# Optimization experiments

Hardware: AMD Instinct MI355X
Metric: run time of the kernel (lower is better)

## Reference

```python
import jax, jax.numpy as jnp
import numpy as np

D, H, S, T, NN, IN_CH, FEAT, SPA, OUT, NL, FF, E = 512, 8, 64, 32, 512, 32, 64, 32, 32, 4, 2048, 16384
NEG = 0.2  # leaky relu negative slope (GATv2 default and alpha)

def _ln(x, g, b):
    m = x.mean(-1, keepdims=True)
    v = ((x - m) ** 2).mean(-1, keepdims=True)
    return (x - m) / jnp.sqrt(v + 1e-5) * g + b

def _posenc(L):
    pos = jnp.arange(L, dtype=jnp.float32)[:, None]
    div = jnp.exp(-jnp.log(10000.0) * jnp.arange(0, D, 2, dtype=jnp.float32) / D)
    pe = jnp.zeros((L, D), jnp.float32)
    pe = pe.at[:, 0::2].set(jnp.sin(pos * div)).at[:, 1::2].set(jnp.cos(pos * div))
    return pe[:, None, :]  # (L,1,D), seq-first

def _mha(xq, xkv, wqkv, bqkv, wo, bo, mask=None):
    Lq, N, _ = xq.shape
    Lk = xkv.shape[0]
    dh = D // H
    wq, wk, wv = jnp.split(wqkv, 3, axis=1)
    bq, bk, bv = jnp.split(bqkv, 3)
    q = (xq @ wq + bq).reshape(Lq, N, H, dh)
    k = (xkv @ wk + bk).reshape(Lk, N, H, dh)
    v = (xkv @ wv + bv).reshape(Lk, N, H, dh)
    s = jnp.einsum('qnhd,knhd->nhqk', q, k) / jnp.sqrt(jnp.float32(dh))
    if mask is not None:
        s = s + mask
    a = jax.nn.softmax(s, -1)
    o = jnp.einsum('nhqk,knhd->qnhd', a, v).reshape(Lq, N, D)
    return o @ wo + bo

def _gatv2(x, wl, wr, bl, br, att, bias, e_src, e_dst):
    # GATv2: e_ij = a . leakyrelu(Wl x_j + Wr x_i); softmax over incoming edges of i; out_i = sum alpha_ij Wl x_j
    n = x.shape[0]
    h, c = att.shape
    xl = (x @ wl + bl).reshape(n, h, c)
    xr = (x @ wr + br).reshape(n, h, c)
    z = jax.nn.leaky_relu(xl[e_src] + xr[e_dst], NEG)   # (E,H,C)
    e = jnp.einsum('ehc,hc->eh', z, att)                # (E,H)
    m = jax.lax.stop_gradient(jax.ops.segment_max(e, e_dst, num_segments=n))
    ex = jnp.exp(e - m[e_dst])
    den = jax.ops.segment_sum(ex, e_dst, num_segments=n)
    alpha = ex / den[e_dst]
    out = jax.ops.segment_sum(alpha[..., None] * xl[e_src], e_dst, num_segments=n)
    return out.reshape(n, h * c) + bias

def _fwd(src, tgt, w_enc_in, b_enc_in, w_dec_in, b_dec_in, w_map, b_map,
         enc_qkv_w, enc_qkv_b, enc_out_w, enc_out_b, enc_ff1_w, enc_ff1_b, enc_ff2_w, enc_ff2_b,
         enc_ln1_g, enc_ln1_b, enc_ln2_g, enc_ln2_b, enc_fn_g, enc_fn_b,
         dec_sa_qkv_w, dec_sa_qkv_b, dec_sa_out_w, dec_sa_out_b,
         dec_ca_qkv_w, dec_ca_qkv_b, dec_ca_out_w, dec_ca_out_b,
         dec_ff1_w, dec_ff1_b, dec_ff2_w, dec_ff2_b,
         dec_ln1_g, dec_ln1_b, dec_ln2_g, dec_ln2_b, dec_ln3_g, dec_ln3_b, dec_fn_g, dec_fn_b,
         g1_wl, g1_wr, g1_bl, g1_br, g1_att, g1_bias,
         g2_wl, g2_wr, g2_bl, g2_br, g2_att, g2_bias,
         edge_index):
    # temporal transformer (eval mode, dropout off), seq-first (L, N, D)
    x = src @ w_enc_in + b_enc_in + _posenc(S)
    for i in range(NL):  # post-norm encoder, relu FFN (nn.TransformerEncoderLayer defaults)
        a = _mha(x, x, enc_qkv_w[i], enc_qkv_b[i], enc_out_w[i], enc_out_b[i])
        x = _ln(x + a, enc_ln1_g[i], enc_ln1_b[i])
        f = jax.nn.relu(x @ enc_ff1_w[i] + enc_ff1_b[i]) @ enc_ff2_w[i] + enc_ff2_b[i]
        x = _ln(x + f, enc_ln2_g[i], enc_ln2_b[i])
    mem = _ln(x, enc_fn_g, enc_fn_b)
    causal = jnp.triu(jnp.full((T, T), -1e9, jnp.float32), k=1)
    y = tgt @ w_dec_in + b_dec_in + _posenc(T)
    for i in range(NL):
        a = _mha(y, y, dec_sa_qkv_w[i], dec_sa_qkv_b[i], dec_sa_out_w[i], dec_sa_out_b[i], causal)
        y = _ln(y + a, dec_ln1_g[i], dec_ln1_b[i])
        a = _mha(y, mem, dec_ca_qkv_w[i], dec_ca_qkv_b[i], dec_ca_out_w[i], dec_ca_out_b[i])
        y = _ln(y + a, dec_ln2_g[i], dec_ln2_b[i])
        f = jax.nn.relu(y @ dec_ff1_w[i] + dec_ff1_b[i]) @ dec_ff2_w[i] + dec_ff2_b[i]
        y = _ln(y + f, dec_ln3_g[i], dec_ln3_b[i])
    y = _ln(y, dec_fn_g, dec_fn_b) @ w_map + b_map  # (T, N, FEAT)
    e_src, e_dst = edge_index[0], edge_index[1]
    def spatial(xt):  # two-layer GATv2 per time step, then elu (concat=True branch)
        h1 = _gatv2(xt, g1_wl, g1_wr, g1_bl, g1_br, g1_att, g1_bias, e_src, e_dst)
        h2 = _gatv2(h1, g2_wl, g2_wr, g2_bl, g2_br, g2_att, g2_bias, e_src, e_dst)
        return jax.nn.elu(h2)
    g = jax.vmap(spatial)(y)  # (T, N, H*OUT)
    return jax.nn.relu(g)


def setup_inputs():
    ks = iter(jax.random.split(jax.random.key(0), 100))
    def w(shape, s=0.05):
        return jax.random.normal(next(ks), shape, jnp.float32) * s
    inp = {}
    inp['src'] = jax.random.normal(next(ks), (S, NN, IN_CH), jnp.float32)
    inp['tgt'] = jax.random.normal(next(ks), (T, NN, FEAT), jnp.float32)
    inp['w_enc_in'] = w((IN_CH, D)); inp['b_enc_in'] = jnp.zeros((D,))
    inp['w_dec_in'] = w((FEAT, D)); inp['b_dec_in'] = jnp.zeros((D,))
    inp['w_map'] = w((D, FEAT)); inp['b_map'] = jnp.zeros((FEAT,))
    inp['enc_qkv_w'] = w((NL, D, 3 * D)); inp['enc_qkv_b'] = jnp.zeros((NL, 3 * D))
    inp['enc_out_w'] = w((NL, D, D)); inp['enc_out_b'] = jnp.zeros((NL, D))
    inp['enc_ff1_w'] = w((NL, D, FF)); inp['enc_ff1_b'] = jnp.zeros((NL, FF))
    inp['enc_ff2_w'] = w((NL, FF, D)); inp['enc_ff2_b'] = jnp.zeros((NL, D))
    inp['enc_ln1_g'] = jnp.ones((NL, D)); inp['enc_ln1_b'] = jnp.zeros((NL, D))
    inp['enc_ln2_g'] = jnp.ones((NL, D)); inp['enc_ln2_b'] = jnp.zeros((NL, D))
    inp['enc_fn_g'] = jnp.ones((D,)); inp['enc_fn_b'] = jnp.zeros((D,))
    inp['dec_sa_qkv_w'] = w((NL, D, 3 * D)); inp['dec_sa_qkv_b'] = jnp.zeros((NL, 3 * D))
    inp['dec_sa_out_w'] = w((NL, D, D)); inp['dec_sa_out_b'] = jnp.zeros((NL, D))
    inp['dec_ca_qkv_w'] = w((NL, D, 3 * D)); inp['dec_ca_qkv_b'] = jnp.zeros((NL, 3 * D))
    inp['dec_ca_out_w'] = w((NL, D, D)); inp['dec_ca_out_b'] = jnp.zeros((NL, D))
    inp['dec_ff1_w'] = w((NL, D, FF)); inp['dec_ff1_b'] = jnp.zeros((NL, FF))
    inp['dec_ff2_w'] = w((NL, FF, D)); inp['dec_ff2_b'] = jnp.zeros((NL, D))
    inp['dec_ln1_g'] = jnp.ones((NL, D)); inp['dec_ln1_b'] = jnp.zeros((NL, D))
    inp['dec_ln2_g'] = jnp.ones((NL, D)); inp['dec_ln2_b'] = jnp.zeros((NL, D))
    inp['dec_ln3_g'] = jnp.ones((NL, D)); inp['dec_ln3_b'] = jnp.zeros((NL, D))
    inp['dec_fn_g'] = jnp.ones((D,)); inp['dec_fn_b'] = jnp.zeros((D,))
    inp['g1_wl'] = w((FEAT, H * SPA)); inp['g1_wr'] = w((FEAT, H * SPA))
    inp['g1_bl'] = jnp.zeros((H * SPA,)); inp['g1_br'] = jnp.zeros((H * SPA,))
    inp['g1_att'] = w((H, SPA), 0.1); inp['g1_bias'] = jnp.zeros((H * SPA,))
    inp['g2_wl'] = w((H * SPA, H * OUT)); inp['g2_wr'] = w((H * SPA, H * OUT))
    inp['g2_bl'] = jnp.zeros((H * OUT,)); inp['g2_br'] = jnp.zeros((H * OUT,))
    inp['g2_att'] = w((H, OUT), 0.1); inp['g2_bias'] = jnp.zeros((H * OUT,))
    inp['edge_index'] = jax.random.randint(next(ks), (2, E), 0, NN)
    return inp


def reference(src, tgt, w_enc_in, b_enc_in, w_dec_in, b_dec_in, w_map, b_map,
              enc_qkv_w, enc_qkv_b, enc_out_w, enc_out_b, enc_ff1_w, enc_ff1_b, enc_ff2_w, enc_ff2_b,
              enc_ln1_g, enc_ln1_b, enc_ln2_g, enc_ln2_b, enc_fn_g, enc_fn_b,
              dec_sa_qkv_w, dec_sa_qkv_b, dec_sa_out_w, dec_sa_out_b,
              dec_ca_qkv_w, dec_ca_qkv_b, dec_ca_out_w, dec_ca_out_b,
              dec_ff1_w, dec_ff1_b, dec_ff2_w, dec_ff2_b,
              dec_ln1_g, dec_ln1_b, dec_ln2_g, dec_ln2_b, dec_ln3_g, dec_ln3_b, dec_fn_g, dec_fn_b,
              g1_wl, g1_wr, g1_bl, g1_br, g1_att, g1_bias,
              g2_wl, g2_wr, g2_bl, g2_br, g2_att, g2_bias,
              edge_index):
    return _fwd(src, tgt, w_enc_in, b_enc_in, w_dec_in, b_dec_in, w_map, b_map,
                enc_qkv_w, enc_qkv_b, enc_out_w, enc_out_b, enc_ff1_w, enc_ff1_b, enc_ff2_w, enc_ff2_b,
                enc_ln1_g, enc_ln1_b, enc_ln2_g, enc_ln2_b, enc_fn_g, enc_fn_b,
                dec_sa_qkv_w, dec_sa_qkv_b, dec_sa_out_w, dec_sa_out_b,
                dec_ca_qkv_w, dec_ca_qkv_b, dec_ca_out_w, dec_ca_out_b,
                dec_ff1_w, dec_ff1_b, dec_ff2_w, dec_ff2_b,
                dec_ln1_g, dec_ln1_b, dec_ln2_g, dec_ln2_b, dec_ln3_g, dec_ln3_b, dec_fn_g, dec_fn_b,
                g1_wl, g1_wr, g1_bl, g1_br, g1_att, g1_bias,
                g2_wl, g2_wr, g2_bl, g2_br, g2_att, g2_bias,
                edge_index)
```

## Files before the change

kernel.cpp:

```cpp
#include <hip/hip_runtime.h>
#include <hip/hip_bf16.h>

#define NHEAD 8
#define SLEN 64
#define TLEN 32
#define NNODE 512
#define NEDGE 16384
#define NLAYER 4

typedef __attribute__((ext_vector_type(8))) __bf16 bf16x8;
typedef __attribute__((ext_vector_type(4))) __bf16 bf16x4;
typedef __attribute__((ext_vector_type(4))) float  f32x4;

__device__ __forceinline__ void gload16(const void* g, void* l)
{
    __builtin_amdgcn_global_load_lds(
        (const __attribute__((address_space(1))) void*)g,
        (__attribute__((address_space(3))) void*)l, 16, 0, 0);
}

template<int BN>
__global__ __launch_bounds__(256) void gemm_bf16(
    const __bf16* __restrict__ A, int lda,
    const __bf16* __restrict__ Bt, int ldb,
    const float* __restrict__ bias,
    float* __restrict__ Cf, __bf16* __restrict__ Cb, int ldc,
    int M, int N, int K, int outMode)
{
    constexpr int FM = (BN == 128) ? 4 : 2;
    __shared__ __bf16 As[128 * 64];
    __shared__ __bf16 Bs[BN * 64];
    const int tid  = threadIdx.x;
    const int wid  = tid >> 6;
    const int lane = tid & 63;
    const int wr = (BN == 128) ? (wid >> 1) : wid;
    const int wc = (BN == 128) ? (wid & 1) : 0;
    const int m0 = blockIdx.y * 128, n0 = blockIdx.x * BN;

    const int srow = wid * 8 + (lane >> 3);
    const int scol = (lane & 7) * 8;
    const int lr = lane & 15;
    const int kg = (lane >> 4) * 8;

    f32x4 acc[FM][4];
    #pragma unroll
    for (int m = 0; m < FM; ++m)
        #pragma unroll
        for (int n = 0; n < 4; ++n)
            acc[m][n] = (f32x4){0.0f, 0.0f, 0.0f, 0.0f};

    for (int k0 = 0; k0 < K; k0 += 64) {
        #pragma unroll
        for (int g = 0; g < 4; ++g) {
            const __bf16* ga = A + (size_t)(m0 + g * 32 + srow) * lda + k0 + scol;
            gload16(ga, &As[(g * 32 + wid * 8) * 64]);
        }
        #pragma unroll
        for (int g = 0; g < BN / 32; ++g) {
            const __bf16* gb = Bt + (size_t)(n0 + g * 32 + srow) * ldb + k0 + scol;
            gload16(gb, &Bs[(g * 32 + wid * 8) * 64]);
        }
        __syncthreads();
        #pragma unroll
        for (int kk = 0; kk < 64; kk += 32) {
            bf16x8 fa[FM], fb[4];
            #pragma unroll
            for (int m = 0; m < FM; ++m)
                fa[m] = *reinterpret_cast<const bf16x8*>(
                    &As[(wr * (16 * FM) + m * 16 + lr) * 64 + kk + kg]);
            #pragma unroll
            for (int n = 0; n < 4; ++n)
                fb[n] = *reinterpret_cast<const bf16x8*>(
                    &Bs[(wc * 64 + n * 16 + lr) * 64 + kk + kg]);
            #pragma unroll
            for (int m = 0; m < FM; ++m)
                #pragma unroll
                for (int n = 0; n < 4; ++n)
                    acc[m][n] = __builtin_amdgcn_mfma_f32_16x16x32_bf16(
                        fa[m], fb[n], acc[m][n], 0, 0, 0);
        }
        __syncthreads();
    }

    const int cr = (lane >> 4) * 4;
    const int cc = lane & 15;
    #pragma unroll
    for (int n = 0; n < 4; ++n) {
        const int gcol = n0 + wc * 64 + n * 16 + cc;
        const float bb = bias[gcol];
        #pragma unroll
        for (int m = 0; m < FM; ++m) {
            #pragma unroll
            for (int j = 0; j < 4; ++j) {
                const int grow = m0 + wr * (16 * FM) + m * 16 + cr + j;
                float v = acc[m][n][j] + bb;
                if (outMode == 1 || outMode == 2) v = fmaxf(v, 0.0f);
                if (outMode >= 2) Cb[(size_t)grow * ldc + gcol] = (__bf16)v;
                else              Cf[(size_t)grow * ldc + gcol] = v;
            }
        }
    }
}

__global__ __launch_bounds__(256) void gemm_bias(
    const float* __restrict__ A, int lda,
    const float* __restrict__ B, int ldb,
    const float* __restrict__ bias,
    float* __restrict__ C, int ldc,
    int M, int N, int K, int relu)
{
    __shared__ float As[16][68];
    __shared__ float Bs[16][68];
    const int tid = threadIdx.x;
    const int tx = tid & 15, ty = tid >> 4;
    const int m0 = blockIdx.y * 64, n0 = blockIdx.x * 64;
    const int liA_m = tid >> 2;
    const int liA_k = (tid & 3) * 4;
    const int liB_n = (tid & 15) * 4;
    const int liB_k = tid >> 4;
    float acc[4][4] = {};
    for (int k0 = 0; k0 < K; k0 += 16) {
        float4 av = *reinterpret_cast<const float4*>(&A[(size_t)(m0 + liA_m) * lda + k0 + liA_k]);
        float4 bv = *reinterpret_cast<const float4*>(&B[(size_t)(k0 + liB_k) * ldb + n0 + liB_n]);
        As[liA_k + 0][liA_m] = av.x;
        As[liA_k + 1][liA_m] = av.y;
        As[liA_k + 2][liA_m] = av.z;
        As[liA_k + 3][liA_m] = av.w;
        *reinterpret_cast<float4*>(&Bs[liB_k][liB_n]) = bv;
        __syncthreads();
        #pragma unroll
        for (int kk = 0; kk < 16; ++kk) {
            float4 a4 = *reinterpret_cast<const float4*>(&As[kk][ty * 4]);
            float4 b4 = *reinterpret_cast<const float4*>(&Bs[kk][tx * 4]);
            float a[4] = {a4.x, a4.y, a4.z, a4.w};
            float b[4] = {b4.x, b4.y, b4.z, b4.w};
            #pragma unroll
            for (int i = 0; i < 4; ++i)
                #pragma unroll
                for (int j = 0; j < 4; ++j)
                    acc[i][j] += a[i] * b[j];
        }
        __syncthreads();
    }
    #pragma unroll
    for (int i = 0; i < 4; ++i) {
        const int m = m0 + ty * 4 + i;
        #pragma unroll
        for (int j = 0; j < 4; ++j) {
            const int n = n0 + tx * 4 + j;
            float v = acc[i][j] + bias[n];
            if (relu) v = fmaxf(v, 0.0f);
            C[(size_t)m * ldc + n] = v;
        }
    }
}

__global__ __launch_bounds__(256) void transpose_w(
    const float* __restrict__ in, __bf16* __restrict__ out, int K, int N)
{
    __shared__ __bf16 t[32][33];
    const int l = blockIdx.z;
    in  += (size_t)l * K * N;
    out += (size_t)l * K * N;
    const int k0 = blockIdx.y * 32, n0 = blockIdx.x * 32;
    const int tx = threadIdx.x & 31, ty = threadIdx.x >> 5;
    #pragma unroll
    for (int i = 0; i < 32; i += 8)
        t[ty + i][tx] = (__bf16)in[(size_t)(k0 + ty + i) * N + n0 + tx];
    __syncthreads();
    #pragma unroll
    for (int i = 0; i < 32; i += 8)
        out[(size_t)(n0 + ty + i) * K + k0 + tx] = t[tx][ty + i];
}

__global__ __launch_bounds__(256) void conv_bf16(
    const float* __restrict__ in, __bf16* __restrict__ out, int total4)
{
    const int i = blockIdx.x * 256 + threadIdx.x;
    if (i >= total4) return;
    const float4 v = *reinterpret_cast<const float4*>(&in[(size_t)i * 4]);
    bf16x4 w;
    w[0] = (__bf16)v.x; w[1] = (__bf16)v.y; w[2] = (__bf16)v.z; w[3] = (__bf16)v.w;
    *reinterpret_cast<bf16x4*>(&out[(size_t)i * 4]) = w;
}

__global__ __launch_bounds__(256) void permute_in(
    const float* __restrict__ in, float* __restrict__ out, int L, int CH, int total)
{
    const int idx = blockIdx.x * 256 + threadIdx.x;
    if (idx >= total) return;
    const int c = idx % CH;
    const int r = idx / CH;
    const int n = r & 511;
    const int l = r >> 9;
    out[((size_t)n * L + l) * CH + c] = in[idx];
}

__global__ __launch_bounds__(256) void permute_F(
    const float* __restrict__ in, float* __restrict__ out)
{
    const int idx = blockIdx.x * 256 + threadIdx.x;
    const int c = idx & 63;
    const int r = idx >> 6;
    const int n = r >> 5;
    const int t = r & 31;
    out[((size_t)(t * 512 + n)) * 64 + c] = in[idx];
}

template<int LQ, int LK, bool CAUSAL>
__global__ __launch_bounds__(64) void attn_mfma(
    const __bf16* __restrict__ Q, int ldq,
    const __bf16* __restrict__ Kp, int ldk,
    const __bf16* __restrict__ Vp, int ldv,
    __bf16* __restrict__ O, int ldo)
{
    constexpr int QF = LQ / 16, KF = LK / 16;
    constexpr int PSTR = LK + 8;
    __shared__ __bf16 Vt[64 * PSTR];
    __shared__ __bf16 Ps[LQ * PSTR];
    const int n = blockIdx.x >> 3;
    const int h = blockIdx.x & 7;
    const int lane = threadIdx.x;
    const int lr = lane & 15;
    const int g4 = lane >> 4;
    const int kg = g4 * 8;

    if (lane < LK) {
        #pragma unroll
        for (int j = 0; j < 8; ++j) {
            bf16x8 vv = *reinterpret_cast<const bf16x8*>(
                &Vp[(size_t)(n * LK + lane) * ldv + h * 64 + j * 8]);
            #pragma unroll
            for (int e = 0; e < 8; ++e)
                Vt[(j * 8 + e) * PSTR + lane] = vv[e];
        }
    }

    f32x4 s[QF][KF];
    #pragma unroll
    for (int qi = 0; qi < QF; ++qi)
        #pragma unroll
        for (int ki = 0; ki < KF; ++ki)
            s[qi][ki] = (f32x4){0.0f, 0.0f, 0.0f, 0.0f};
    #pragma unroll
    for (int kk = 0; kk < 64; kk += 32) {
        bf16x8 fa[QF], fb[KF];
        #pragma unroll
        for (int qi = 0; qi < QF; ++qi)
            fa[qi] = *reinterpret_cast<const bf16x8*>(
                &Q[(size_t)(n * LQ + qi * 16 + lr) * ldq + h * 64 + kk + kg]);
        #pragma unroll
        for (int ki = 0; ki < KF; ++ki)
            fb[ki] = *reinterpret_cast<const bf16x8*>(
                &Kp[(size_t)(n * LK + ki * 16 + lr) * ldk + h * 64 + kk + kg]);
        #pragma unroll
        for (int qi = 0; qi < QF; ++qi)
            #pragma unroll
            for (int ki = 0; ki < KF; ++ki)
                s[qi][ki] = __builtin_amdgcn_mfma_f32_16x16x32_bf16(fa[qi], fb[ki], s[qi][ki], 0, 0, 0);
    }

    float inv_s[QF][4];
    #pragma unroll
    for (int qi = 0; qi < QF; ++qi) {
        #pragma unroll
        for (int j = 0; j < 4; ++j) {
            const int row = qi * 16 + g4 * 4 + j;
            float mx = -1e30f;
            #pragma unroll
            for (int ki = 0; ki < KF; ++ki) {
                float v = s[qi][ki][j] * 0.125f;
                if (CAUSAL) { const int col = ki * 16 + lr; if (col > row) v = -1e30f; }
                s[qi][ki][j] = v;
                mx = fmaxf(mx, v);
            }
            #pragma unroll
            for (int d = 1; d < 16; d <<= 1) mx = fmaxf(mx, __shfl_xor(mx, d));
            float sum = 0.0f;
            #pragma unroll
            for (int ki = 0; ki < KF; ++ki) {
                const float p = __expf(s[qi][ki][j] - mx);
                s[qi][ki][j] = p;
                sum += p;
            }
            #pragma unroll
            for (int d = 1; d < 16; d <<= 1) sum += __shfl_xor(sum, d);
            inv_s[qi][j] = 1.0f / sum;
            #pragma unroll
            for (int ki = 0; ki < KF; ++ki)
                Ps[row * PSTR + ki * 16 + lr] = (__bf16)s[qi][ki][j];
        }
    }
    __syncthreads();

    f32x4 o[QF][4];
    #pragma unroll
    for (int qi = 0; qi < QF; ++qi)
        #pragma unroll
        for (int di = 0; di < 4; ++di)
            o[qi][di] = (f32x4){0.0f, 0.0f, 0.0f, 0.0f};
    #pragma unroll
    for (int kk = 0; kk < LK; kk += 32) {
        bf16x8 fa[QF], fb[4];
        #pragma unroll
        for (int qi = 0; qi < QF; ++qi)
            fa[qi] = *reinterpret_cast<const bf16x8*>(&Ps[(qi * 16 + lr) * PSTR + kk + kg]);
        #pragma unroll
        for (int di = 0; di < 4; ++di)
            fb[di] = *reinterpret_cast<const bf16x8*>(&Vt[(di * 16 + lr) * PSTR + kk + kg]);
        #pragma unroll
        for (int qi = 0; qi < QF; ++qi)
            #pragma unroll
            for (int di = 0; di < 4; ++di)
                o[qi][di] = __builtin_amdgcn_mfma_f32_16x16x32_bf16(fa[qi], fb[di], o[qi][di], 0, 0, 0);
    }
    #pragma unroll
    for (int qi = 0; qi < QF; ++qi)
        #pragma unroll
        for (int di = 0; di < 4; ++di)
            #pragma unroll
            for (int j = 0; j < 4; ++j) {
                const int row = qi * 16 + g4 * 4 + j;
                O[(size_t)(n * LQ + row) * ldo + h * 64 + di * 16 + lr] =
                    (__bf16)(o[qi][di][j] * inv_s[qi][j]);
            }
}

template<bool HASR, bool F32OUT>
__global__ __launch_bounds__(256) void ln_bf16(
    const __bf16* __restrict__ X, const __bf16* __restrict__ Rb,
    const float* __restrict__ g, const float* __restrict__ b,
    __bf16* __restrict__ outb, float* __restrict__ outf, int ntok)
{
    const int wid = threadIdx.x >> 6, lane = threadIdx.x & 63;
    const int row = blockIdx.x * 4 + wid;
    if (row >= ntok) return;
    const size_t base = (size_t)row * 512;
    const int c0 = lane * 8;
    const bf16x8 xv = *reinterpret_cast<const bf16x8*>(&X[base + c0]);
    float v[8];
    float s = 0.0f;
    if (HASR) {
        const bf16x8 rv = *reinterpret_cast<const bf16x8*>(&Rb[base + c0]);
        #pragma unroll
        for (int j = 0; j < 8; ++j) { v[j] = (float)xv[j] + (float)rv[j]; s += v[j]; }
    } else {
        #pragma unroll
        for (int j = 0; j < 8; ++j) { v[j] = (float)xv[j]; s += v[j]; }
    }
    #pragma unroll
    for (int d = 32; d >= 1; d >>= 1) s += __shfl_xor(s, d, 64);
    const float mean = s * (1.0f / 512.0f);
    float vs = 0.0f;
    #pragma unroll
    for (int j = 0; j < 8; ++j) { const float d = v[j] - mean; vs += d * d; }
    #pragma unroll
    for (int d = 32; d >= 1; d >>= 1) vs += __shfl_xor(vs, d, 64);
    const float rstd = rsqrtf(vs * (1.0f / 512.0f) + 1e-5f);
    const float4 g0 = *reinterpret_cast<const float4*>(&g[c0]);
    const float4 g1 = *reinterpret_cast<const float4*>(&g[c0 + 4]);
    const float4 b0 = *reinterpret_cast<const float4*>(&b[c0]);
    const float4 b1 = *reinterpret_cast<const float4*>(&b[c0 + 4]);
    const float gg[8] = {g0.x, g0.y, g0.z, g0.w, g1.x, g1.y, g1.z, g1.w};
    const float bb[8] = {b0.x, b0.y, b0.z, b0.w, b1.x, b1.y, b1.z, b1.w};
    if (F32OUT) {
        f32x4 o0, o1;
        #pragma unroll
        for (int j = 0; j < 4; ++j) o0[j] = (v[j] - mean) * rstd * gg[j] + bb[j];
        #pragma unroll
        for (int j = 0; j < 4; ++j) o1[j] = (v[4 + j] - mean) * rstd * gg[4 + j] + bb[4 + j];
        *reinterpret_cast<f32x4*>(&outf[base + c0]) = o0;
        *reinterpret_cast<f32x4*>(&outf[base + c0 + 4]) = o1;
    } else {
        bf16x8 w;
        #pragma unroll
        for (int j = 0; j < 8; ++j) w[j] = (__bf16)((v[j] - mean) * rstd * gg[j] + bb[j]);
        *reinterpret_cast<bf16x8*>(&outb[base + c0]) = w;
    }
}

__global__ __launch_bounds__(256) void add_posenc(float* __restrict__ x, int L, int total)
{
    const int idx = blockIdx.x * 256 + threadIdx.x;
    if (idx >= total) return;
    const int d = idx & 511;
    const int row = idx >> 9;
    const int l = row % L;
    const int i2 = d & ~1;
    const float freq = expf(-9.210340371976184f * (float)i2 / 512.0f);
    const float a = (float)l * freq;
    x[idx] += (d & 1) ? cosf(a) : sinf(a);
}

__global__ void zero_ints(int* __restrict__ p, int n)
{
    const int i = blockIdx.x * 256 + threadIdx.x;
    if (i < n) p[i] = 0;
}

__global__ void count_deg(const int* __restrict__ edst, int* __restrict__ deg)
{
    const int e = blockIdx.x * 256 + threadIdx.x;
    if (e < NEDGE) atomicAdd(&deg[edst[e]], 1);
}

__global__ void scan512(const int* __restrict__ deg, int* __restrict__ off)
{
    __shared__ int s[512];
    const int tid = threadIdx.x;
    s[tid] = deg[tid];
    __syncthreads();
    for (int d = 1; d < 512; d <<= 1) {
        const int t = (tid >= d) ? s[tid - d] : 0;
        __syncthreads();
        s[tid] += t;
        __syncthreads();
    }
    off[tid + 1] = s[tid];
    if (tid == 0) off[0] = 0;
}

__global__ void fill_eid(const int* __restrict__ edst, const int* __restrict__ off,
                         int* __restrict__ cur, int* __restrict__ eid)
{
    const int e = blockIdx.x * 256 + threadIdx.x;
    if (e < NEDGE) {
        const int d = edst[e];
        const int pos = off[d] + atomicAdd(&cur[d], 1);
        eid[pos] = e;
    }
}

template<bool FINAL>
__global__ __launch_bounds__(256) void gatv2_kernel(
    const float* __restrict__ xl, const float* __restrict__ xr,
    const float* __restrict__ att, const float* __restrict__ bias,
    const int* __restrict__ off, const int* __restrict__ eid,
    const int* __restrict__ esrc,
    float* __restrict__ outf, float* __restrict__ outd)
{
    const int blk = blockIdx.x;
    const int i = blk & (NNODE - 1);
    const int t = blk >> 9;
    const int tid = threadIdx.x;
    const float xrv = xr[(size_t)blk * 256 + tid];
    const float av = att[tid];
    const int e0 = off[i], e1 = off[i + 1];
    float m = -1e30f, den = 0.0f, acc = 0.0f;
    for (int idx = e0; idx < e1; ++idx) {
        const int e = eid[idx];
        const int s = esrc[e];
        const float xlv = xl[((size_t)(t * 512 + s)) * 256 + tid];
        float z = xlv + xrv;
        z = (z > 0.0f) ? z : 0.2f * z;
        float w = z * av;
        #pragma unroll
        for (int d = 16; d >= 1; d >>= 1) w += __shfl_xor(w, d, 32);
        const float mn = fmaxf(m, w);
        const float sc = __expf(m - mn);
        const float p  = __expf(w - mn);
        den = den * sc + p;
        acc = acc * sc + p * xlv;
        m = mn;
    }
    float o = (den > 0.0f) ? acc / den : 0.0f;
    o += bias[tid];
    if (FINAL) {
        o = fmaxf(o, 0.0f);
        outd[(size_t)blk * 256 + tid] = o;
    } else {
        outf[(size_t)blk * 256 + tid] = o;
    }
}

extern "C" void kernel_launch(void* const* d_in, const int* in_sizes, int n_in,
                              void* d_out, int out_size, void* d_ws, size_t ws_size,
                              hipStream_t stream)
{
    const float* src       = (const float*)d_in[0];
    const float* tgt       = (const float*)d_in[1];
    const float* w_enc_in  = (const float*)d_in[2];
    const float* b_enc_in  = (const float*)d_in[3];
    const float* w_dec_in  = (const float*)d_in[4];
    const float* b_dec_in  = (const float*)d_in[5];
    const float* w_map     = (const float*)d_in[6];
    const float* b_map     = (const float*)d_in[7];
    const float* enc_qkv_w = (const float*)d_in[8];
    const float* enc_qkv_b = (const float*)d_in[9];
    const float* enc_out_w = (const float*)d_in[10];
    const float* enc_out_b = (const float*)d_in[11];
    const float* enc_ff1_w = (const float*)d_in[12];
    const float* enc_ff1_b = (const float*)d_in[13];
    const float* enc_ff2_w = (const float*)d_in[14];
    const float* enc_ff2_b = (const float*)d_in[15];
    const float* enc_ln1_g = (const float*)d_in[16];
    const float* enc_ln1_b = (const float*)d_in[17];
    const float* enc_ln2_g = (const float*)d_in[18];
    const float* enc_ln2_b = (const float*)d_in[19];
    const float* enc_fn_g  = (const float*)d_in[20];
    const float* enc_fn_b  = (const float*)d_in[21];
    const float* dec_sa_qkv_w = (const float*)d_in[22];
    const float* dec_sa_qkv_b = (const float*)d_in[23];
    const float* dec_sa_out_w = (const float*)d_in[24];
    const float* dec_sa_out_b = (const float*)d_in[25];
    const float* dec_ca_qkv_w = (const float*)d_in[26];
    const float* dec_ca_qkv_b = (const float*)d_in[27];
    const float* dec_ca_out_w = (const float*)d_in[28];
    const float* dec_ca_out_b = (const float*)d_in[29];
    const float* dec_ff1_w = (const float*)d_in[30];
    const float* dec_ff1_b = (const float*)d_in[31];
    const float* dec_ff2_w = (const float*)d_in[32];
    const float* dec_ff2_b = (const float*)d_in[33];
    const float* dec_ln1_g = (const float*)d_in[34];
    const float* dec_ln1_b = (const float*)d_in[35];
    const float* dec_ln2_g = (const float*)d_in[36];
    const float* dec_ln2_b = (const float*)d_in[37];
    const float* dec_ln3_g = (const float*)d_in[38];
    const float* dec_ln3_b = (const float*)d_in[39];
    const float* dec_fn_g  = (const float*)d_in[40];
    const float* dec_fn_b  = (const float*)d_in[41];
    const float* g1_wl   = (const float*)d_in[42];
    const float* g1_wr   = (const float*)d_in[43];
    const float* g1_bl   = (const float*)d_in[44];
    const float* g1_br   = (const float*)d_in[45];
    const float* g1_att  = (const float*)d_in[46];
    const float* g1_bias = (const float*)d_in[47];
    const float* g2_wl   = (const float*)d_in[48];
    const float* g2_wr   = (const float*)d_in[49];
    const float* g2_bl   = (const float*)d_in[50];
    const float* g2_br   = (const float*)d_in[51];
    const float* g2_att  = (const float*)d_in[52];
    const float* g2_bias = (const float*)d_in[53];
    const int*   edge_index = (const int*)d_in[54];
    const int* esrc = edge_index;
    const int* edst = edge_index + NEDGE;

    float* wsf = (float*)d_ws;
    __bf16* Xb = (__bf16*)wsf;
    __bf16* Yb = (__bf16*)(wsf + 8388608);
    float*  Rf = wsf + 12582912;
    float*  Mf = wsf + 20971520;
    float*  Wf = wsf + 29360128;
    float*  F  = wsf + 37748736;
    int* ipool = (int*)(wsf + 38797312);
    int* deg = ipool;
    int* off = deg + 512;
    int* cur = off + 516;
    int* eid = cur + 512;
    __bf16* Rb16 = (__bf16*)Rf;
    __bf16* Mb16 = (__bf16*)Mf;
    __bf16* Wb   = (__bf16*)Wf;

    auto gemm = [&](const float* A, int lda, const float* B, int ldb, const float* bias,
                    float* Cc, int ldc, int M, int N, int K, int relu) {
        dim3 grid((unsigned)(N / 64), (unsigned)(M / 64));
        gemm_bias<<<grid, 256, 0, stream>>>(A, lda, B, ldb, bias, Cc, ldc, M, N, K, relu);
    };
    auto gemmT = [&](const __bf16* A, int lda, const __bf16* Bt, int ldb,
                     const float* bias, float* Cf, __bf16* Cb, int ldc,
                     int M, int N, int K, int mode) {
        dim3 grid((unsigned)(N / 128), (unsigned)(M / 128));
        gemm_bf16<128><<<grid, 256, 0, stream>>>(A, lda, Bt, ldb, bias, Cf, Cb, ldc, M, N, K, mode);
    };
    auto gemmT64 = [&](const __bf16* A, int lda, const __bf16* Bt, int ldb,
                       const float* bias, float* Cf, __bf16* Cb, int ldc,
                       int M, int N, int K, int mode) {
        dim3 grid((unsigned)(N / 64), (unsigned)(M / 128));
        gemm_bf16<64><<<grid, 256, 0, stream>>>(A, lda, Bt, ldb, bias, Cf, Cb, ldc, M, N, K, mode);
    };
    auto tw = [&](const float* w, __bf16* o, int K, int N) {
        dim3 g((unsigned)(N / 32), (unsigned)(K / 32), NLAYER);
        transpose_w<<<g, 256, 0, stream>>>(w, o, K, N);
    };

    zero_ints<<<8, 256, 0, stream>>>(ipool, 512 + 516 + 512);
    count_deg<<<NEDGE / 256, 256, 0, stream>>>(edst, deg);
    scan512<<<1, 512, 0, stream>>>(deg, off);
    fill_eid<<<NEDGE / 256, 256, 0, stream>>>(edst, off, cur, eid);

    {
        float* src_nm = Wf;
        float* Xtmp = Rf;
        permute_in<<<4096, 256, 0, stream>>>(src, src_nm, SLEN, 32, 32768 * 32);
        gemm(src_nm, 32, w_enc_in, 512, b_enc_in, Xtmp, 512, 32768, 512, 32, 0);
        add_posenc<<<(32768 * 512) / 256, 256, 0, stream>>>(Xtmp, SLEN, 32768 * 512);
        conv_bf16<<<16384, 256, 0, stream>>>(Xtmp, Xb, 32768 * 128);
        float* tgt_nm = Wf;
        float* Ytmp = Rf;
        permute_in<<<4096, 256, 0, stream>>>(tgt, tgt_nm, TLEN, 64, 16384 * 64);
        gemm(tgt_nm, 64, w_dec_in, 512, b_dec_in, Ytmp, 512, 16384, 512, 64, 0);
        add_posenc<<<(16384 * 512) / 256, 256, 0, stream>>>(Ytmp, TLEN, 16384 * 512);
        conv_bf16<<<8192, 256, 0, stream>>>(Ytmp, Yb, 16384 * 128);
    }

    __bf16* WeQkv = Wb + 0;
    __bf16* WeOut = Wb + 3145728;
    __bf16* WeFf1 = Wb + 4194304;
    __bf16* WeFf2 = Wb + 8388608;
    tw(enc_qkv_w, WeQkv, 512, 1536);
    tw(enc_out_w, WeOut, 512, 512);
    tw(enc_ff1_w, WeFf1, 512, 2048);
    tw(enc_ff2_w, WeFf2, 2048, 512);

    for (int i = 0; i < NLAYER; ++i) {
        for (int c = 0; c < 4; ++c) {
            gemmT(Xb + (size_t)c * 8192 * 512, 512, WeQkv + (size_t)i * 786432, 512,
                  enc_qkv_b + (size_t)i * 1536, nullptr, Rb16, 1536, 8192, 1536, 512, 3);
            attn_mfma<64, 64, false><<<1024, 64, 0, stream>>>(
                Rb16, 1536, Rb16 + 512, 1536, Rb16 + 1024, 1536,
                Mb16 + (size_t)c * 8192 * 512, 512);
        }
        gemmT(Mb16, 512, WeOut + (size_t)i * 262144, 512, enc_out_b + (size_t)i * 512,
              nullptr, Rb16, 512, 32768, 512, 512, 3);
        ln_bf16<true, false><<<8192, 256, 0, stream>>>(Xb, Rb16,
            enc_ln1_g + (size_t)i * 512, enc_ln1_b + (size_t)i * 512, Xb, nullptr, 32768);
        for (int s = 0; s < 4; ++s) {
            gemmT(Xb + (size_t)s * 8192 * 512, 512, WeFf1 + (size_t)i * 1048576, 512,
                  enc_ff1_b + (size_t)i * 2048, nullptr, Mb16, 2048, 8192, 2048, 512, 2);
            gemmT64(Mb16, 2048, WeFf2 + (size_t)i * 1048576, 2048,
                    enc_ff2_b + (size_t)i * 512, nullptr, Rb16 + (size_t)s * 8192 * 512, 512,
                    8192, 512, 2048, 3);
        }
        ln_bf16<true, false><<<8192, 256, 0, stream>>>(Xb, Rb16,
            enc_ln2_g + (size_t)i * 512, enc_ln2_b + (size_t)i * 512, Xb, nullptr, 32768);
    }
    ln_bf16<false, false><<<8192, 256, 0, stream>>>(Xb, nullptr, enc_fn_g, enc_fn_b,
                                                    Xb, nullptr, 32768);

    __bf16* WdSaQkv = Wb + 0;
    __bf16* WdSaOut = Wb + 3145728;
    __bf16* WdCaQkv = Wb + 4194304;
    __bf16* WdCaOut = Wb + 7340032;
    __bf16* WdFf1   = Wb + 8388608;
    __bf16* WdFf2   = Wb + 12582912;
    tw(dec_sa_qkv_w, WdSaQkv, 512, 1536);
    tw(dec_sa_out_w, WdSaOut, 512, 512);
    tw(dec_ca_qkv_w, WdCaQkv, 512, 1536);
    tw(dec_ca_out_w, WdCaOut, 512, 512);
    tw(dec_ff1_w,    WdFf1,   512, 2048);
    tw(dec_ff2_w,    WdFf2,   2048, 512);

    __bf16* ObD  = Mb16;
    __bf16* QbC  = Mb16;
    __bf16* ObCA = (__bf16*)(Mf + 2097152);
    for (int i = 0; i < NLAYER; ++i) {
        for (int c = 0; c < 2; ++c) {
            gemmT(Yb + (size_t)c * 8192 * 512, 512, WdSaQkv + (size_t)i * 786432, 512,
                  dec_sa_qkv_b + (size_t)i * 1536, nullptr, Rb16, 1536, 8192, 1536, 512, 3);
            attn_mfma<32, 32, true><<<2048, 64, 0, stream>>>(
                Rb16, 1536, Rb16 + 512, 1536, Rb16 + 1024, 1536,
                ObD + (size_t)c * 8192 * 512, 512);
        }
        gemmT64(ObD, 512, WdSaOut + (size_t)i * 262144, 512, dec_sa_out_b + (size_t)i * 512,
                nullptr, Rb16, 512, 16384, 512, 512, 3);
        ln_bf16<true, false><<<4096, 256, 0, stream>>>(Yb, Rb16,
            dec_ln1_g + (size_t)i * 512, dec_ln1_b + (size_t)i * 512, Yb, nullptr, 16384);
        for (int c = 0; c < 2; ++c) {
            gemmT64(Yb + (size_t)c * 8192 * 512, 512, WdCaQkv + (size_t)i * 786432, 512,
                    dec_ca_qkv_b + (size_t)i * 1536, nullptr, QbC, 512, 8192, 512, 512, 3);
            gemmT(Xb + (size_t)c * 16384 * 512, 512, WdCaQkv + (size_t)i * 786432 + 262144, 512,
                  dec_ca_qkv_b + (size_t)i * 1536 + 512, nullptr, Rb16, 1024, 16384, 1024, 512, 3);
            attn_mfma<32, 64, false><<<2048, 64, 0, stream>>>(
                QbC, 512, Rb16, 1024, Rb16 + 512, 1024,
                ObCA + (size_t)c * 8192 * 512, 512);
        }
        gemmT64(ObCA, 512, WdCaOut + (size_t)i * 262144, 512, dec_ca_out_b + (size_t)i * 512,
                nullptr, Rb16, 512, 16384, 512, 512, 3);
        ln_bf16<true, false><<<4096, 256, 0, stream>>>(Yb, Rb16,
            dec_ln2_g + (size_t)i * 512, dec_ln2_b + (size_t)i * 512, Yb, nullptr, 16384);
        for (int s = 0; s < 2; ++s) {
            gemmT(Yb + (size_t)s * 8192 * 512, 512, WdFf1 + (size_t)i * 1048576, 512,
                  dec_ff1_b + (size_t)i * 2048, nullptr, Mb16, 2048, 8192, 2048, 512, 2);
            gemmT64(Mb16, 2048, WdFf2 + (size_t)i * 1048576, 2048,
                    dec_ff2_b + (size_t)i * 512, nullptr, Rb16 + (size_t)s * 8192 * 512, 512,
                    8192, 512, 2048, 3);
        }
        ln_bf16<true, false><<<4096, 256, 0, stream>>>(Yb, Rb16,
            dec_ln3_g + (size_t)i * 512, dec_ln3_b + (size_t)i * 512, Yb, nullptr, 16384);
    }
    float* Yf = Rf;
    ln_bf16<false, true><<<4096, 256, 0, stream>>>(Yb, nullptr, dec_fn_g, dec_fn_b,
                                                   nullptr, Yf, 16384);

    gemm(Yf, 512, w_map, 64, b_map, F, 64, 16384, 64, 512, 0);
    float* Ft = Wf;
    permute_F<<<4096, 256, 0, stream>>>(F, Ft);

    float* G  = Mf;
    float* Hb = Mf + 4194304;
    float* Ib = Wf + 1048576;
    gemm(Ft, 64, g1_wl, 256, g1_bl, G,  256, 16384, 256, 64, 0);
    gemm(Ft, 64, g1_wr, 256, g1_br, Hb, 256, 16384, 256, 64, 0);
    gatv2_kernel<false><<<16384, 256, 0, stream>>>(G, Hb, g1_att, g1_bias, off, eid, esrc, Ib, nullptr);
    gemm(Ib, 256, g2_wl, 256, g2_bl, G,  256, 16384, 256, 256, 0);
    gemm(Ib, 256, g2_wr, 256, g2_br, Hb, 256, 16384, 256, 256, 0);
    gatv2_kernel<true><<<16384, 256, 0, stream>>>(G, Hb, g2_att, g2_bias, off, eid, esrc,
                                                  nullptr, (float*)d_out);
}
```

Measured before the change: 4.698 ms.

## Fuse residual adds into GEMM epilogues and move tail GEMMs to bf16 MFMA

Adds an optional residual input to the bf16 MFMA GEMM epilogue, so the out-projection and FF2 GEMMs write x+f(x) in place and the layernorms no longer read a separate residual buffer. FFN chunks are enlarged (encoder 2 chunks of 16384 rows, decoder a single pass), and the cross-attention Q projection becomes one GEMM per layer. The final map projection and the GATv2 linear layers now use transposed bf16 weights with the MFMA GEMM instead of the fp32 tiled GEMM. This trades extra bf16 rounding in the GNN tail for fewer launches and less memory traffic.

```diff
diff --git a/kernel.cpp b/kernel.cpp
--- a/kernel.cpp
+++ b/kernel.cpp
@@ -24,6 +24,7 @@
     const __bf16* __restrict__ A, int lda,
     const __bf16* __restrict__ Bt, int ldb,
     const float* __restrict__ bias,
+    const __bf16* __restrict__ Res,
     float* __restrict__ Cf, __bf16* __restrict__ Cb, int ldc,
     int M, int N, int K, int outMode)
 {
@@ -94,6 +95,7 @@
             for (int j = 0; j < 4; ++j) {
                 const int grow = m0 + wr * (16 * FM) + m * 16 + cr + j;
                 float v = acc[m][n][j] + bb;
+                if (Res) v += (float)Res[(size_t)grow * ldc + gcol];
                 if (outMode == 1 || outMode == 2) v = fmaxf(v, 0.0f);
                 if (outMode >= 2) Cb[(size_t)grow * ldc + gcol] = (__bf16)v;
                 else              Cf[(size_t)grow * ldc + gcol] = v;
@@ -197,9 +199,10 @@
 }
 
 __global__ __launch_bounds__(256) void permute_F(
-    const float* __restrict__ in, float* __restrict__ out)
+    const __bf16* __restrict__ in, __bf16* __restrict__ out)
 {
     const int idx = blockIdx.x * 256 + threadIdx.x;
+    if (idx >= 16384 * 64) return;
     const int c = idx & 63;
     const int r = idx >> 6;
     const int n = r >> 5;
@@ -437,7 +440,7 @@
     const float* __restrict__ att, const float* __restrict__ bias,
     const int* __restrict__ off, const int* __restrict__ eid,
     const int* __restrict__ esrc,
-    float* __restrict__ outf, float* __restrict__ outd)
+    __bf16* __restrict__ outb16, float* __restrict__ outd)
 {
     const int blk = blockIdx.x;
     const int i = blk & (NNODE - 1);
@@ -469,7 +472,7 @@
         o = fmaxf(o, 0.0f);
         outd[(size_t)blk * 256 + tid] = o;
     } else {
-        outf[(size_t)blk * 256 + tid] = o;
+        outb16[(size_t)blk * 256 + tid] = (__bf16)o;
     }
 }
 
@@ -550,6 +553,7 @@
     __bf16* Rb16 = (__bf16*)Rf;
     __bf16* Mb16 = (__bf16*)Mf;
     __bf16* Wb   = (__bf16*)Wf;
+    __bf16* midb = (__bf16*)Rf;
 
     auto gemm = [&](const float* A, int lda, const float* B, int ldb, const float* bias,
                     float* Cc, int ldc, int M, int N, int K, int relu) {
@@ -557,19 +561,19 @@
         gemm_bias<<<grid, 256, 0, stream>>>(A, lda, B, ldb, bias, Cc, ldc, M, N, K, relu);
     };
     auto gemmT = [&](const __bf16* A, int lda, const __bf16* Bt, int ldb,
-                     const float* bias, float* Cf, __bf16* Cb, int ldc,
+                     const float* bias, const __bf16* Res, float* Cf, __bf16* Cb, int ldc,
                      int M, int N, int K, int mode) {
         dim3 grid((unsigned)(N / 128), (unsigned)(M / 128));
-        gemm_bf16<128><<<grid, 256, 0, stream>>>(A, lda, Bt, ldb, bias, Cf, Cb, ldc, M, N, K, mode);
+        gemm_bf16<128><<<grid, 256, 0, stream>>>(A, lda, Bt, ldb, bias, Res, Cf, Cb, ldc, M, N, K, mode);
     };
     auto gemmT64 = [&](const __bf16* A, int lda, const __bf16* Bt, int ldb,
-                       const float* bias, float* Cf, __bf16* Cb, int ldc,
+                       const float* bias, const __bf16* Res, float* Cf, __bf16* Cb, int ldc,
                        int M, int N, int K, int mode) {
         dim3 grid((unsigned)(N / 64), (unsigned)(M / 128));
-        gemm_bf16<64><<<grid, 256, 0, stream>>>(A, lda, Bt, ldb, bias, Cf, Cb, ldc, M, N, K, mode);
+        gemm_bf16<64><<<grid, 256, 0, stream>>>(A, lda, Bt, ldb, bias, Res, Cf, Cb, ldc, M, N, K, mode);
     };
-    auto tw = [&](const float* w, __bf16* o, int K, int N) {
-        dim3 g((unsigned)(N / 32), (unsigned)(K / 32), NLAYER);
+    auto tw = [&](const float* w, __bf16* o, int K, int N, int L) {
+        dim3 g((unsigned)(N / 32), (unsigned)(K / 32), (unsigned)L);
         transpose_w<<<g, 256, 0, stream>>>(w, o, K, N);
     };
 
@@ -597,31 +601,31 @@
     __bf16* WeOut = Wb + 3145728;
     __bf16* WeFf1 = Wb + 4194304;
     __bf16* WeFf2 = Wb + 8388608;
-    tw(enc_qkv_w, WeQkv, 512, 1536);
-    tw(enc_out_w, WeOut, 512, 512);
-    tw(enc_ff1_w, WeFf1, 512, 2048);
-    tw(enc_ff2_w, WeFf2, 2048, 512);
+    tw(enc_qkv_w, WeQkv, 512, 1536, NLAYER);
+    tw(enc_out_w, WeOut, 512, 512, NLAYER);
+    tw(enc_ff1_w, WeFf1, 512, 2048, NLAYER);
+    tw(enc_ff2_w, WeFf2, 2048, 512, NLAYER);
 
     for (int i = 0; i < NLAYER; ++i) {
         for (int c = 0; c < 4; ++c) {
             gemmT(Xb + (size_t)c * 8192 * 512, 512, WeQkv + (size_t)i * 786432, 512,
-                  enc_qkv_b + (size_t)i * 1536, nullptr, Rb16, 1536, 8192, 1536, 512, 3);
+                  enc_qkv_b + (size_t)i * 1536, nullptr, nullptr, Rb16, 1536, 8192, 1536, 512, 3);
             attn_mfma<64, 64, false><<<1024, 64, 0, stream>>>(
                 Rb16, 1536, Rb16 + 512, 1536, Rb16 + 1024, 1536,
                 Mb16 + (size_t)c * 8192 * 512, 512);
         }
         gemmT(Mb16, 512, WeOut + (size_t)i * 262144, 512, enc_out_b + (size_t)i * 512,
-              nullptr, Rb16, 512, 32768, 512, 512, 3);
-        ln_bf16<true, false><<<8192, 256, 0, stream>>>(Xb, Rb16,
+              Xb, nullptr, Xb, 512, 32768, 512, 512, 3);
+        ln_bf16<false, false><<<8192, 256, 0, stream>>>(Xb, nullptr,
             enc_ln1_g + (size_t)i * 512, enc_ln1_b + (size_t)i * 512, Xb, nullptr, 32768);
-        for (int s = 0; s < 4; ++s) {
-            gemmT(Xb + (size_t)s * 8192 * 512, 512, WeFf1 + (size_t)i * 1048576, 512,
-                  enc_ff1_b + (size_t)i * 2048, nullptr, Mb16, 2048, 8192, 2048, 512, 2);
-            gemmT64(Mb16, 2048, WeFf2 + (size_t)i * 1048576, 2048,
-                    enc_ff2_b + (size_t)i * 512, nullptr, Rb16 + (size_t)s * 8192 * 512, 512,
-                    8192, 512, 2048, 3);
-        }
-        ln_bf16<true, false><<<8192, 256, 0, stream>>>(Xb, Rb16,
+        for (int s = 0; s < 2; ++s) {
+            gemmT(Xb + (size_t)s * 16384 * 512, 512, WeFf1 + (size_t)i * 1048576, 512,
+                  enc_ff1_b + (size_t)i * 2048, nullptr, nullptr, midb, 2048, 16384, 2048, 512, 2);
+            gemmT64(midb, 2048, WeFf2 + (size_t)i * 1048576, 2048,
+                    enc_ff2_b + (size_t)i * 512, Xb + (size_t)s * 16384 * 512,
+                    nullptr, Xb + (size_t)s * 16384 * 512, 512, 16384, 512, 2048, 3);
+        }
+        ln_bf16<false, false><<<8192, 256, 0, stream>>>(Xb, nullptr,
             enc_ln2_g + (size_t)i * 512, enc_ln2_b + (size_t)i * 512, Xb, nullptr, 32768);
     }
     ln_bf16<false, false><<<8192, 256, 0, stream>>>(Xb, nullptr, enc_fn_g, enc_fn_b,
@@ -633,67 +637,76 @@
     __bf16* WdCaOut = Wb + 7340032;
     __bf16* WdFf1   = Wb + 8388608;
     __bf16* WdFf2   = Wb + 12582912;
-    tw(dec_sa_qkv_w, WdSaQkv, 512, 1536);
-    tw(dec_sa_out_w, WdSaOut, 512, 512);
-    tw(dec_ca_qkv_w, WdCaQkv, 512, 1536);
-    tw(dec_ca_out_w, WdCaOut, 512, 512);
-    tw(dec_ff1_w,    WdFf1,   512, 2048);
-    tw(dec_ff2_w,    WdFf2,   2048, 512);
+    tw(dec_sa_qkv_w, WdSaQkv, 512, 1536, NLAYER);
+    tw(dec_sa_out_w, WdSaOut, 512, 512, NLAYER);
+    tw(dec_ca_qkv_w, WdCaQkv, 512, 1536, NLAYER);
+    tw(dec_ca_out_w, WdCaOut, 512, 512, NLAYER);
+    tw(dec_ff1_w,    WdFf1,   512, 2048, NLAYER);
+    tw(dec_ff2_w,    WdFf2,   2048, 512, NLAYER);
 
     __bf16* ObD  = Mb16;
     __bf16* QbC  = Mb16;
-    __bf16* ObCA = (__bf16*)(Mf + 2097152);
+    __bf16* ObCA = (__bf16*)(Mf + 4194304);
     for (int i = 0; i < NLAYER; ++i) {
         for (int c = 0; c < 2; ++c) {
             gemmT(Yb + (size_t)c * 8192 * 512, 512, WdSaQkv + (size_t)i * 786432, 512,
-                  dec_sa_qkv_b + (size_t)i * 1536, nullptr, Rb16, 1536, 8192, 1536, 512, 3);
+                  dec_sa_qkv_b + (size_t)i * 1536, nullptr, nullptr, Rb16, 1536, 8192, 1536, 512, 3);
             attn_mfma<32, 32, true><<<2048, 64, 0, stream>>>(
                 Rb16, 1536, Rb16 + 512, 1536, Rb16 + 1024, 1536,
                 ObD + (size_t)c * 8192 * 512, 512);
         }
         gemmT64(ObD, 512, WdSaOut + (size_t)i * 262144, 512, dec_sa_out_b + (size_t)i * 512,
-                nullptr, Rb16, 512, 16384, 512, 512, 3);
-        ln_bf16<true, false><<<4096, 256, 0, stream>>>(Yb, Rb16,
+                Yb, nullptr, Yb, 512, 16384, 512, 512, 3);
+        ln_bf16<false, false><<<4096, 256, 0, stream>>>(Yb, nullptr,
             dec_ln1_g + (size_t)i * 512, dec_ln1_b + (size_t)i * 512, Yb, nullptr, 16384);
+        gemmT64(Yb, 512, WdCaQkv + (size_t)i * 786432, 512,
+                dec_ca_qkv_b + (size_t)i * 1536, nullptr, nullptr, QbC, 512, 16384, 512, 512, 3);
         for (int c = 0; c < 2; ++c) {
-            gemmT64(Yb + (size_t)c * 8192 * 512, 512, WdCaQkv + (size_t)i * 786432, 512,
-                    dec_ca_qkv_b + (size_t)i * 1536, nullptr, QbC, 512, 8192, 512, 512, 3);
             gemmT(Xb + (size_t)c * 16384 * 512, 512, WdCaQkv + (size_t)i * 786432 + 262144, 512,
-                  dec_ca_qkv_b + (size_t)i * 1536 + 512, nullptr, Rb16, 1024, 16384, 1024, 512, 3);
+                  dec_ca_qkv_b + (size_t)i * 1536 + 512, nullptr, nullptr, Rb16, 1024, 16384, 1024, 512, 3);
             attn_mfma<32, 64, false><<<2048, 64, 0, stream>>>(
-                QbC, 512, Rb16, 1024, Rb16 + 512, 1024,
+                QbC + (size_t)c * 8192 * 512, 512, Rb16, 1024, Rb16 + 512, 1024,
                 ObCA + (size_t)c * 8192 * 512, 512);
         }
         gemmT64(ObCA, 512, WdCaOut + (size_t)i * 262144, 512, dec_ca_out_b + (size_t)i * 512,
-                nullptr, Rb16, 512, 16384, 512, 512, 3);
-        ln_bf16<true, false><<<4096, 256, 0, stream>>>(Yb, Rb16,
+                Yb, nullptr, Yb, 512, 16384, 512, 512, 3);
+        ln_bf16<false, false><<<4096, 256, 0, stream>>>(Yb, nullptr,
             dec_ln2_g + (size_t)i * 512, dec_ln2_b + (size_t)i * 512, Yb, nullptr, 16384);
-        for (int s = 0; s < 2; ++s) {
-            gemmT(Yb + (size_t)s * 8192 * 512, 512, WdFf1 + (size_t)i * 1048576, 512,
-                  dec_ff1_b + (size_t)i * 2048, nullptr, Mb16, 2048, 8192, 2048, 512, 2);
-            gemmT64(Mb16, 2048, WdFf2 + (size_t)i * 1048576, 2048,
-                    dec_ff2_b + (size_t)i * 512, nullptr, Rb16 + (size_t)s * 8192 * 512, 512,
-                    8192, 512, 2048, 3);
-        }
-        ln_bf16<true, false><<<4096, 256, 0, stream>>>(Yb, Rb16,
+        gemmT(Yb, 512, WdFf1 + (size_t)i * 1048576, 512,
+              dec_ff1_b + (size_t)i * 2048, nullptr, nullptr, midb, 2048, 16384, 2048, 512, 2);
+        gemmT64(midb, 2048, WdFf2 + (size_t)i * 1048576, 2048,
+                dec_ff2_b + (size_t)i * 512, Yb, nullptr, Yb, 512, 16384, 512, 2048, 3);
+        ln_bf16<false, false><<<4096, 256, 0, stream>>>(Yb, nullptr,
             dec_ln3_g + (size_t)i * 512, dec_ln3_b + (size_t)i * 512, Yb, nullptr, 16384);
     }
-    float* Yf = Rf;
-    ln_bf16<false, true><<<4096, 256, 0, stream>>>(Yb, nullptr, dec_fn_g, dec_fn_b,
-                                                   nullptr, Yf, 16384);
-
-    gemm(Yf, 512, w_map, 64, b_map, F, 64, 16384, 64, 512, 0);
-    float* Ft = Wf;
-    permute_F<<<4096, 256, 0, stream>>>(F, Ft);
+    ln_bf16<false, false><<<4096, 256, 0, stream>>>(Yb, nullptr, dec_fn_g, dec_fn_b,
+                                                    Yb, nullptr, 16384);
+
+    __bf16* Wmapt = Wb;
+    __bf16* G1wlT = Wb + 32768;
+    __bf16* G1wrT = Wb + 49152;
+    __bf16* G2wlT = Wb + 65536;
+    __bf16* G2wrT = Wb + 131072;
+    __bf16* Ftb   = Wb + 196608;
+    __bf16* Ibb   = Wb + 1245184;
+    tw(w_map, Wmapt, 512, 64, 1);
+    tw(g1_wl, G1wlT, 64, 256, 1);
+    tw(g1_wr, G1wrT, 64, 256, 1);
+    tw(g2_wl, G2wlT, 256, 256, 1);
+    tw(g2_wr, G2wrT, 256, 256, 1);
+
+    __bf16* Fb16 = (__bf16*)F;
+    gemmT64(Yb, 512, Wmapt, 512, b_map, nullptr, nullptr, Fb16, 64, 16384, 64, 512, 3);
+    permute_F<<<4096, 256, 0, stream>>>(Fb16, Ftb);
 
     float* G  = Mf;
     float* Hb = Mf + 4194304;
-    float* Ib = Wf + 1048576;
-    gemm(Ft, 64, g1_wl, 256, g1_bl, G,  256, 16384, 256, 64, 0);
-    gemm(Ft, 64, g1_wr, 256, g1_br, Hb, 256, 16384, 256, 64, 0);
-    gatv2_kernel<false><<<16384, 256, 0, stream>>>(G, Hb, g1_att, g1_bias, off, eid, esrc, Ib, nullptr);
-    gemm(Ib, 256, g2_wl, 256, g2_bl, G,  256, 16384, 256, 256, 0);
-    gemm(Ib, 256, g2_wr, 256, g2_br, Hb, 256, 16384, 256, 256, 0);
+    gemmT64(Ftb, 64, G1wlT, 64, g1_bl, nullptr, G,  nullptr, 256, 16384, 256, 64, 0);
+    gemmT64(Ftb, 64, G1wrT, 64, g1_br, nullptr, Hb, nullptr, 256, 16384, 256, 64, 0);
+    gatv2_kernel<false><<<16384, 256, 0, stream>>>(G, Hb, g1_att, g1_bias, off, eid, esrc,
+                                                   Ibb, nullptr);
+    gemmT64(Ibb, 256, G2wlT, 256, g2_bl, nullptr, G,  nullptr, 256, 16384, 256, 256, 0);
+    gemmT64(Ibb, 256, G2wrT, 256, g2_br, nullptr, Hb, nullptr, 256, 16384, 256, 256, 0);
     gatv2_kernel<true><<<16384, 256, 0, stream>>>(G, Hb, g2_att, g2_bias, off, eid, esrc,
                                                   nullptr, (float*)d_out);
 }
```

Measured after the change: 4.839 ms. +3.0%, slower.
